# Kernel tuning notes

Measured on AMD Instinct MI355X. Metric: run time of the kernel, lower is better.

The kernel has to match this reference:

```python
import jax, jax.numpy as jnp
import numpy as np

DIM = 768
NUM_HEADS = 12
HEAD_DIM = DIM // NUM_HEADS
SCALE = HEAD_DIM ** -0.5


def setup_inputs() -> dict:
    key = jax.random.key(0)
    k_x, k_qw, k_qb, k_pw, k_pb = jax.random.split(key, 5)
    B, N = 4, 2048
    x = jax.random.normal(k_x, (B, N, DIM), dtype=jnp.float32)
    s = 1.0 / np.sqrt(DIM)
    qkv_w = jax.random.normal(k_qw, (3 * DIM, DIM), dtype=jnp.float32) * s
    qkv_b = jax.random.normal(k_qb, (3 * DIM,), dtype=jnp.float32) * 0.02
    proj_w = jax.random.normal(k_pw, (DIM, DIM), dtype=jnp.float32) * s
    proj_b = jax.random.normal(k_pb, (DIM,), dtype=jnp.float32) * 0.02
    return {"x": x, "qkv_w": qkv_w, "qkv_b": qkv_b, "proj_w": proj_w, "proj_b": proj_b}


def reference(x, qkv_w, qkv_b, proj_w, proj_b):
    B, N, D = x.shape
    H, Hd = NUM_HEADS, HEAD_DIM
    # qkv linear: [B,N,3D] -> [3,B,H,N,Hd]
    qkv = (x @ qkv_w.T + qkv_b).reshape(B, N, 3, H, Hd).transpose(2, 0, 3, 1, 4)
    q, k, v = qkv[0], qkv[1], qkv[2]
    scores = jnp.einsum("bhnd,bhmd->bhnm", q, k) * SCALE  # [B,H,N,N]
    attn = jax.nn.softmax(scores, axis=-1)
    out = jnp.einsum("bhnm,bhmd->bhnd", attn, v)  # [B,H,N,Hd]
    out = out.transpose(0, 2, 1, 3).reshape(B, N, D)
    return out @ proj_w.T + proj_b
```

## Files before the change

### kernel.cpp

```cpp
#include <hip/hip_runtime.h>

#define SEQ 2048
#define NB 4
#define NH 12
#define DHEAD 64
#define DMODEL 768
#define D3 2304
#define MTOT 8192
#define QSCALE 0.18033688011112042f

typedef float f4v __attribute__((ext_vector_type(4)));
typedef float fl4 __attribute__((ext_vector_type(4)));
typedef short s8v __attribute__((ext_vector_type(8)));
typedef __bf16 b8v __attribute__((ext_vector_type(8)));
typedef unsigned int ui4 __attribute__((ext_vector_type(4)));
typedef unsigned int ui2 __attribute__((ext_vector_type(2)));
typedef unsigned short us4 __attribute__((ext_vector_type(4)));

#define GLDS16(g, l)                                                            \
  __builtin_amdgcn_global_load_lds(                                             \
      (const __attribute__((address_space(1))) void*)(g),                       \
      (__attribute__((address_space(3))) void*)(l), 16, 0, 0)

__device__ inline float fast_exp2(float x) {
#if __has_builtin(__builtin_amdgcn_exp2f)
  return __builtin_amdgcn_exp2f(x);
#else
  float r;
  asm("v_exp_f32 %0, %1" : "=v"(r) : "v"(x));
  return r;
#endif
}

template <typename T>
__device__ inline auto mfma_try(T a, T b, f4v c, int)
    -> decltype(__builtin_amdgcn_mfma_f32_16x16x32_bf16(a, b, c, 0, 0, 0)) {
  return __builtin_amdgcn_mfma_f32_16x16x32_bf16(a, b, c, 0, 0, 0);
}
template <typename T>
__device__ inline f4v mfma_try(T a, T b, f4v c, long) {
  return __builtin_amdgcn_mfma_f32_16x16x32_bf16(
      __builtin_bit_cast(b8v, a), __builtin_bit_cast(b8v, b), c, 0, 0, 0);
}
__device__ inline f4v mfma16(s8v a, s8v b, f4v c) { return mfma_try(a, b, c, 0); }

__device__ inline unsigned short f2bf(float f) {
  union { float f; unsigned u; } v; v.f = f;
  unsigned r = v.u + 0x7FFFu + ((v.u >> 16) & 1u);
  return (unsigned short)(r >> 16);
}

__device__ inline unsigned pack2(float a, float b) {
  unsigned ua = __builtin_bit_cast(unsigned, a) + 0x8000u;
  unsigned ub = __builtin_bit_cast(unsigned, b) + 0x8000u;
  return __builtin_amdgcn_perm(ub, ua, 0x07060302u);
}

__device__ inline unsigned cvtpk2(float a, float b) {
  unsigned r;
  asm("v_cvt_pk_bf16_f32 %0, %1, %2" : "=v"(r) : "v"(a), "v"(b));
  return r;
}

#define NX4 1572864
#define NW14 442368
#define NW24 147456
__global__ void k_cvt(const float* __restrict__ x, const float* __restrict__ w1,
                      const float* __restrict__ w2, unsigned short* __restrict__ ox,
                      unsigned short* __restrict__ o1, unsigned short* __restrict__ o2) {
  int i = blockIdx.x * 256 + threadIdx.x;
  const float* src;
  unsigned short* dst;
  int off;
  if (i < NX4) { src = x; dst = ox; off = i; }
  else if (i < NX4 + NW14) { src = w1; dst = o1; off = i - NX4; }
  else if (i < NX4 + NW14 + NW24) { src = w2; dst = o2; off = i - NX4 - NW14; }
  else return;
  fl4 f = ((const fl4*)src)[off];
  ui2 o = ui2{cvtpk2(f[0], f[1]), cvtpk2(f[2], f[3])};
  ((ui2*)dst)[off] = o;
}

__global__ __launch_bounds__(256, 3) void k_qkv(
    const unsigned short* __restrict__ xb,
    const unsigned short* __restrict__ wb,
    const float* __restrict__ qkv_b,
    unsigned short* __restrict__ outQ,
    unsigned short* __restrict__ outK,
    unsigned short* __restrict__ outV) {
  __shared__ unsigned short As[128 * 64];
  __shared__ unsigned short Bs[128 * 64];
  const int tid = threadIdx.x;
  const int lane = tid & 63;
  const int wave = tid >> 6;
  const int wr = wave >> 1, wc = wave & 1;
  const int lr = lane & 15, lq = lane >> 4;
  const int srow = wave * 8 + (lane >> 3);
  const int scol = ((lane & 7) ^ ((lane >> 3) & 7)) * 8;
  const int swz = (lr & 7);

  const int bid = blockIdx.x;
  const int xcd = bid & 7;
  const int cc = bid >> 3;
  const int tokTile = xcd * 8 + cc / 24;
  const int rsel = cc % 24;

  if (rsel < 12) {
    const int rowBase = rsel * 128;
    const int colBase = tokTile * 128;
    f4v acc[4][4];
#pragma unroll
    for (int i = 0; i < 4; ++i)
#pragma unroll
      for (int j = 0; j < 4; ++j) acc[i][j] = f4v{0.f, 0.f, 0.f, 0.f};

    const unsigned short* Ag0 = wb + (long)(rowBase + srow) * DMODEL + scol;
    const unsigned short* Bg0 = xb + (long)(colBase + srow) * DMODEL + scol;
    unsigned short* Al0 = &As[srow * 64 + (lane & 7) * 8];
    unsigned short* Bl0 = &Bs[srow * 64 + (lane & 7) * 8];

    for (int kt = 0; kt < DMODEL / 64; ++kt) {
#pragma unroll
      for (int p = 0; p < 4; ++p) {
        GLDS16(Ag0 + kt * 64 + p * 32 * DMODEL, Al0 + p * 32 * 64);
        GLDS16(Bg0 + kt * 64 + p * 32 * DMODEL, Bl0 + p * 32 * 64);
      }
      __syncthreads();
#pragma unroll
      for (int ks = 0; ks < 2; ++ks) {
        s8v af[4], bf[4];
#pragma unroll
        for (int i = 0; i < 4; ++i)
          af[i] = *(const s8v*)&As[(wr * 64 + i * 16 + lr) * 64 + ((ks * 4 + lq) ^ swz) * 8];
#pragma unroll
        for (int j = 0; j < 4; ++j)
          bf[j] = *(const s8v*)&Bs[(wc * 64 + j * 16 + lr) * 64 + ((ks * 4 + lq) ^ swz) * 8];
#pragma unroll
        for (int i = 0; i < 4; ++i)
#pragma unroll
          for (int j = 0; j < 4; ++j) acc[i][j] = mfma16(af[i], bf[j], acc[i][j]);
      }
      __syncthreads();
    }

    const int fw = rowBase + wr * 64;
    fl4 bv[4];
#pragma unroll
    for (int i = 0; i < 4; ++i) bv[i] = *(const fl4*)&qkv_b[fw + i * 16 + lq * 4];
    const int isQ = fw < DMODEL;
    const int h = (fw >> 6) % NH;
    unsigned short* outQK = (unsigned short*)(isQ ? outQ : outK);
    const float scl = isQ ? QSCALE : 1.0f;
#pragma unroll
    for (int j = 0; j < 4; ++j) {
      const int ng = colBase + wc * 64 + j * 16 + lr;
      const int b = ng >> 11, nn = ng & 2047;
#pragma unroll
      for (int i = 0; i < 4; ++i) {
        float v0 = (acc[i][j][0] + bv[i][0]) * scl, v1 = (acc[i][j][1] + bv[i][1]) * scl;
        float v2 = (acc[i][j][2] + bv[i][2]) * scl, v3 = (acc[i][j][3] + bv[i][3]) * scl;
        *(ui2*)(outQK + (long)(((b * NH + h) * SEQ) + nn) * DHEAD + (i * 16 + lq * 4)) =
            ui2{cvtpk2(v0, v1), cvtpk2(v2, v3)};
      }
    }
  } else {
    const int rowBase = tokTile * 128;
    const int colBase = (rsel - 12) * 64;
    f4v acc[4][2];
#pragma unroll
    for (int i = 0; i < 4; ++i)
#pragma unroll
      for (int j = 0; j < 2; ++j) acc[i][j] = f4v{0.f, 0.f, 0.f, 0.f};

    const unsigned short* Ag0 = xb + (long)(rowBase + srow) * DMODEL + scol;
    const unsigned short* Bg0 =
        wb + (long)(2 * DMODEL + colBase + srow) * DMODEL + scol;
    unsigned short* Al0 = &As[srow * 64 + (lane & 7) * 8];
    unsigned short* Bl0 = &Bs[srow * 64 + (lane & 7) * 8];

    for (int kt = 0; kt < DMODEL / 64; ++kt) {
#pragma unroll
      for (int p = 0; p < 4; ++p)
        GLDS16(Ag0 + kt * 64 + p * 32 * DMODEL, Al0 + p * 32 * 64);
#pragma unroll
      for (int p = 0; p < 2; ++p)
        GLDS16(Bg0 + kt * 64 + p * 32 * DMODEL, Bl0 + p * 32 * 64);
      __syncthreads();
#pragma unroll
      for (int ks = 0; ks < 2; ++ks) {
        s8v af[4], bf[2];
#pragma unroll
        for (int i = 0; i < 4; ++i)
          af[i] = *(const s8v*)&As[(wr * 64 + i * 16 + lr) * 64 + ((ks * 4 + lq) ^ swz) * 8];
#pragma unroll
        for (int j = 0; j < 2; ++j)
          bf[j] = *(const s8v*)&Bs[(wc * 32 + j * 16 + lr) * 64 + ((ks * 4 + lq) ^ swz) * 8];
#pragma unroll
        for (int i = 0; i < 4; ++i)
#pragma unroll
          for (int j = 0; j < 2; ++j) acc[i][j] = mfma16(af[i], bf[j], acc[i][j]);
      }
      __syncthreads();
    }

#pragma unroll
    for (int j = 0; j < 2; ++j) {
      const int col = colBase + wc * 32 + j * 16 + lr;
      const float bvs = qkv_b[2 * DMODEL + col];
      const int h = col >> 6, hd = col & 63;
#pragma unroll
      for (int i = 0; i < 4; ++i) {
        const int row = rowBase + wr * 64 + i * 16 + lq * 4;
        const int b = row >> 11, n = row & 2047;
        const int bq = (n >> 2) & 7;
        const int np = (n & ~31) + ((bq & 3) << 3) + ((bq >> 2) << 2);
        float v0 = acc[i][j][0] + bvs, v1 = acc[i][j][1] + bvs;
        float v2 = acc[i][j][2] + bvs, v3 = acc[i][j][3] + bvs;
        *(ui2*)&outV[(long)(((b * NH + h) * DHEAD) + hd) * SEQ + np] =
            ui2{cvtpk2(v0, v1), cvtpk2(v2, v3)};
      }
    }
  }
}

__global__ __launch_bounds__(256, 3) void k_proj(
    const unsigned short* __restrict__ Wp,
    const unsigned short* __restrict__ Xt,
    const float* __restrict__ bias,
    float* __restrict__ outF) {
  __shared__ unsigned short As[128 * 64];
  __shared__ unsigned short Bs[64 * 64];
  const int tid = threadIdx.x;
  const int lane = tid & 63;
  const int wave = tid >> 6;
  const int wr = wave >> 1, wc = wave & 1;
  const int lr = lane & 15, lq = lane >> 4;
  const int srow = wave * 8 + (lane >> 3);
  const int scol = ((lane & 7) ^ ((lane >> 3) & 7)) * 8;
  const int swz = (lr & 7);

  const int bid = blockIdx.x;
  const int xcd = bid & 7;
  const int cc = bid >> 3;
  const int tokTile = xcd * 16 + cc / 6;
  const int rowBase = (cc % 6) * 128;
  const int colBase = tokTile * 64;

  f4v acc[4][2];
#pragma unroll
  for (int i = 0; i < 4; ++i)
#pragma unroll
    for (int j = 0; j < 2; ++j) acc[i][j] = f4v{0.f, 0.f, 0.f, 0.f};

  const unsigned short* Ag0 = Wp + (long)(rowBase + srow) * DMODEL + scol;
  const unsigned short* Bg0 = Xt + (long)(colBase + srow) * DMODEL + scol;
  unsigned short* Al0 = &As[srow * 64 + (lane & 7) * 8];
  unsigned short* Bl0 = &Bs[srow * 64 + (lane & 7) * 8];

  for (int kt = 0; kt < DMODEL / 64; ++kt) {
#pragma unroll
    for (int p = 0; p < 4; ++p)
      GLDS16(Ag0 + kt * 64 + p * 32 * DMODEL, Al0 + p * 32 * 64);
#pragma unroll
    for (int p = 0; p < 2; ++p)
      GLDS16(Bg0 + kt * 64 + p * 32 * DMODEL, Bl0 + p * 32 * 64);
    __syncthreads();
#pragma unroll
    for (int ks = 0; ks < 2; ++ks) {
      s8v af[4], bf[2];
#pragma unroll
      for (int i = 0; i < 4; ++i)
        af[i] = *(const s8v*)&As[(wr * 64 + i * 16 + lr) * 64 + ((ks * 4 + lq) ^ swz) * 8];
#pragma unroll
      for (int j = 0; j < 2; ++j)
        bf[j] = *(const s8v*)&Bs[(wc * 32 + j * 16 + lr) * 64 + ((ks * 4 + lq) ^ swz) * 8];
#pragma unroll
      for (int i = 0; i < 4; ++i)
#pragma unroll
        for (int j = 0; j < 2; ++j) acc[i][j] = mfma16(af[i], bf[j], acc[i][j]);
    }
    __syncthreads();
  }

  const int fw = rowBase + wr * 64;
  fl4 bv[4];
#pragma unroll
  for (int i = 0; i < 4; ++i) bv[i] = *(const fl4*)&bias[fw + i * 16 + lq * 4];
#pragma unroll
  for (int j = 0; j < 2; ++j) {
    const int ng = colBase + wc * 32 + j * 16 + lr;
#pragma unroll
    for (int i = 0; i < 4; ++i) {
      float v0 = acc[i][j][0] + bv[i][0], v1 = acc[i][j][1] + bv[i][1];
      float v2 = acc[i][j][2] + bv[i][2], v3 = acc[i][j][3] + bv[i][3];
      *(fl4*)&outF[(long)ng * DMODEL + fw + i * 16 + lq * 4] = fl4{v0, v1, v2, v3};
    }
  }
}

__global__ __launch_bounds__(256, 3) void k_attn(
    const unsigned short* __restrict__ Q,
    const unsigned short* __restrict__ Kg,
    const unsigned short* __restrict__ Vt,
    unsigned short* __restrict__ Ob) {
  __shared__ unsigned short Ks[2 * 128 * 64];
  __shared__ unsigned short Vs[64 * 128];
  const int tid = threadIdx.x;
  const int lane = tid & 63;
  const int wave = tid >> 6;
  const int lr = lane & 15;
  const int lq = lane >> 4;

  const int bid = blockIdx.x;
  const int xcd = bid & 7;
  const int cc = bid >> 3;
  const int bh = xcd * 6 + cc / 16;
  const int q0 = (cc & 15) * 128;

  const int b = bh / NH, h = bh % NH;
  const unsigned short* Qb = Q + (long)bh * SEQ * DHEAD;
  const unsigned short* Kb = Kg + (long)bh * SEQ * DHEAD;
  const unsigned short* Vb = Vt + (long)bh * DHEAD * SEQ;

  s8v qf[2][2];
#pragma unroll
  for (int i = 0; i < 2; ++i)
#pragma unroll
    for (int ss = 0; ss < 2; ++ss)
      qf[i][ss] = *(const s8v*)(Qb + (q0 + wave * 32 + i * 16 + lr) * DHEAD + ss * 32 + lq * 8);

  f4v o[2][4];
  f4v la[2] = {f4v{0.f, 0.f, 0.f, 0.f}, f4v{0.f, 0.f, 0.f, 0.f}};
  const f4v zc = f4v{0.f, 0.f, 0.f, 0.f};
  const s8v ones = {0x3F80, 0x3F80, 0x3F80, 0x3F80, 0x3F80, 0x3F80, 0x3F80, 0x3F80};
#pragma unroll
  for (int i = 0; i < 2; ++i)
#pragma unroll
    for (int jo = 0; jo < 4; ++jo) o[i][jo] = f4v{0.f, 0.f, 0.f, 0.f};

  const int srow = wave * 8 + (lane >> 3);
  const int scol = ((lane & 7) ^ ((lane >> 3) & 7)) * 8;
  const unsigned short* Kg0 = Kb + (long)srow * DHEAD + scol;
  const int klBase = srow * 64 + (lane & 7) * 8;
  const int swz = (lr & 7);
  const int vdrow = wave * 4 + (lane >> 4);
  const int vchunk = (lane & 15) ^ vdrow;
  const unsigned short* Vg0 = Vb + (long)vdrow * SEQ + vchunk * 8;
  unsigned short* Vl0 = &Vs[vdrow * 128 + (lane & 15) * 8];

#pragma unroll
  for (int p = 0; p < 4; ++p)
    GLDS16(Kg0 + (long)(p * 32) * DHEAD, &Ks[klBase] + p * 32 * 64);
  __syncthreads();

  int cur = 0;
  for (int kt = 0; kt < SEQ / 128; ++kt) {
#pragma unroll
    for (int p = 0; p < 4; ++p)
      GLDS16(Vg0 + (long)(p * 16) * SEQ + kt * 128, Vl0 + p * 16 * 128);
    if (kt + 1 < SEQ / 128) {
#pragma unroll
      for (int p = 0; p < 4; ++p)
        GLDS16(Kg0 + (long)((kt + 1) * 128 + p * 32) * DHEAD,
               &Ks[(cur ^ 1) * (128 * 64) + klBase] + p * 32 * 64);
    }

    const unsigned short* Kc = &Ks[cur * (128 * 64)];
    f4v s[2][8];
    __builtin_amdgcn_s_setprio(1);
#pragma unroll
    for (int t = 0; t < 8; ++t) {
      s8v kf0 = *(const s8v*)&Kc[(t * 16 + lr) * 64 + ((0 * 4 + lq) ^ swz) * 8];
      s8v kf1 = *(const s8v*)&Kc[(t * 16 + lr) * 64 + ((1 * 4 + lq) ^ swz) * 8];
      s[0][t] = mfma16(kf0, qf[0][0], zc);
      s[1][t] = mfma16(kf0, qf[1][0], zc);
      s[0][t] = mfma16(kf1, qf[0][1], s[0][t]);
      s[1][t] = mfma16(kf1, qf[1][1], s[1][t]);
    }
    __builtin_amdgcn_s_setprio(0);

    unsigned pk[2][8][2];
#pragma unroll
    for (int i = 0; i < 2; ++i)
#pragma unroll
      for (int t = 0; t < 4; ++t) {
        float p0 = fast_exp2(s[i][t][0]);
        float p1 = fast_exp2(s[i][t][1]);
        float p2 = fast_exp2(s[i][t][2]);
        float p3 = fast_exp2(s[i][t][3]);
        pk[i][t][0] = cvtpk2(p0, p1);
        pk[i][t][1] = cvtpk2(p2, p3);
      }

    __syncthreads();

#pragma unroll
    for (int ss = 0; ss < 4; ++ss) {
      s8v vf[4];
#pragma unroll
      for (int jo = 0; jo < 4; ++jo)
        vf[jo] = *(const s8v*)&Vs[(jo * 16 + lr) * 128 + ((ss * 4 + lq) ^ lr) * 8];
      __builtin_amdgcn_s_setprio(1);
#pragma unroll
      for (int i = 0; i < 2; ++i) {
        s8v pf = __builtin_bit_cast(
            s8v, ui4{pk[i][2 * ss][0], pk[i][2 * ss][1], pk[i][2 * ss + 1][0], pk[i][2 * ss + 1][1]});
        la[i] = mfma16(ones, pf, la[i]);
#pragma unroll
        for (int jo = 0; jo < 4; ++jo) o[i][jo] = mfma16(vf[jo], pf, o[i][jo]);
      }
      __builtin_amdgcn_s_setprio(0);
      if (ss < 2) {
#pragma unroll
        for (int i = 0; i < 2; ++i)
#pragma unroll
          for (int t = 4 + 2 * ss; t < 6 + 2 * ss; ++t) {
            float p0 = fast_exp2(s[i][t][0]);
            float p1 = fast_exp2(s[i][t][1]);
            float p2 = fast_exp2(s[i][t][2]);
            float p3 = fast_exp2(s[i][t][3]);
            pk[i][t][0] = cvtpk2(p0, p1);
            pk[i][t][1] = cvtpk2(p2, p3);
          }
      }
    }

    __syncthreads();
    cur ^= 1;
  }

  float linv[2];
  linv[0] = 1.0f / la[0][0];
  linv[1] = 1.0f / la[1][0];

#pragma unroll
  for (int i = 0; i < 2; ++i) {
    const long nrow = (long)(b * SEQ + q0 + wave * 32 + i * 16 + lr) * DMODEL;
#pragma unroll
    for (int jo = 0; jo < 4; ++jo) {
      float v0 = o[i][jo][0] * linv[i];
      float v1 = o[i][jo][1] * linv[i];
      float v2 = o[i][jo][2] * linv[i];
      float v3 = o[i][jo][3] * linv[i];
      *(ui2*)(Ob + nrow + h * DHEAD + jo * 16 + lq * 4) = ui2{cvtpk2(v0, v1), cvtpk2(v2, v3)};
    }
  }
}

extern "C" void kernel_launch(void* const* d_in, const int* in_sizes, int n_in,
                              void* d_out, int out_size, void* d_ws, size_t ws_size,
                              hipStream_t stream) {
  (void)in_sizes; (void)n_in; (void)out_size; (void)ws_size;
  const float* x = (const float*)d_in[0];
  const float* qkv_w = (const float*)d_in[1];
  const float* qkv_b = (const float*)d_in[2];
  const float* proj_w = (const float*)d_in[3];
  const float* proj_b = (const float*)d_in[4];
  float* out = (float*)d_out;

  unsigned short* ws = (unsigned short*)d_ws;
  unsigned short* xb = ws;
  unsigned short* wqkvb = xb + 6291456;
  unsigned short* wprjb = wqkvb + 1769472;
  unsigned short* qb = wprjb + 589824;
  unsigned short* kb = qb + 6291456;
  unsigned short* vtb = kb + 6291456;
  unsigned short* aob = vtb + 6291456;

  k_cvt<<<(NX4 + NW14 + NW24 + 255) / 256, 256, 0, stream>>>(
      x, qkv_w, proj_w, xb, wqkvb, wprjb);

  k_qkv<<<1536, 256, 0, stream>>>(xb, wqkvb, qkv_b, qb, kb, vtb);
  k_attn<<<768, 256, 0, stream>>>(qb, kb, vtb, aob);
  k_proj<<<768, 256, 0, stream>>>(wprjb, aob, proj_b, out);
}
```

Measured before the change: 195.3 us.

## Fuse V projection into QK blocks of QKV GEMM sharing the x tile

The QKV kernel used to launch separate blocks for the Q/K part and the V part, and both loaded the same x tile. Each block now computes one 128x128 Q/K tile and also a 128x64 V tile, reusing the x tile already staged in LDS as the A operand for V. This halves the grid and avoids loading x twice. In exchange each block holds more accumulator registers and an extra LDS buffer, which may reduce occupancy below the 3 blocks per CU requested by the launch bounds.

After: 196.6 us. About the same (+0.7%).

```diff
diff --git a/kernel.cpp b/kernel.cpp
--- a/kernel.cpp
+++ b/kernel.cpp
@@ -90,6 +90,7 @@
     unsigned short* __restrict__ outV) {
   __shared__ unsigned short As[128 * 64];
   __shared__ unsigned short Bs[128 * 64];
+  __shared__ unsigned short Cs[64 * 64];
   const int tid = threadIdx.x;
   const int lane = tid & 63;
   const int wave = tid >> 6;
@@ -102,47 +103,68 @@
   const int bid = blockIdx.x;
   const int xcd = bid & 7;
   const int cc = bid >> 3;
-  const int tokTile = xcd * 8 + cc / 24;
-  const int rsel = cc % 24;
-
-  if (rsel < 12) {
-    const int rowBase = rsel * 128;
-    const int colBase = tokTile * 128;
-    f4v acc[4][4];
-#pragma unroll
-    for (int i = 0; i < 4; ++i)
-#pragma unroll
-      for (int j = 0; j < 4; ++j) acc[i][j] = f4v{0.f, 0.f, 0.f, 0.f};
-
-    const unsigned short* Ag0 = wb + (long)(rowBase + srow) * DMODEL + scol;
-    const unsigned short* Bg0 = xb + (long)(colBase + srow) * DMODEL + scol;
-    unsigned short* Al0 = &As[srow * 64 + (lane & 7) * 8];
-    unsigned short* Bl0 = &Bs[srow * 64 + (lane & 7) * 8];
-
-    for (int kt = 0; kt < DMODEL / 64; ++kt) {
-#pragma unroll
-      for (int p = 0; p < 4; ++p) {
-        GLDS16(Ag0 + kt * 64 + p * 32 * DMODEL, Al0 + p * 32 * 64);
-        GLDS16(Bg0 + kt * 64 + p * 32 * DMODEL, Bl0 + p * 32 * 64);
-      }
-      __syncthreads();
-#pragma unroll
-      for (int ks = 0; ks < 2; ++ks) {
-        s8v af[4], bf[4];
-#pragma unroll
-        for (int i = 0; i < 4; ++i)
-          af[i] = *(const s8v*)&As[(wr * 64 + i * 16 + lr) * 64 + ((ks * 4 + lq) ^ swz) * 8];
-#pragma unroll
-        for (int j = 0; j < 4; ++j)
-          bf[j] = *(const s8v*)&Bs[(wc * 64 + j * 16 + lr) * 64 + ((ks * 4 + lq) ^ swz) * 8];
-#pragma unroll
-        for (int i = 0; i < 4; ++i)
-#pragma unroll
-          for (int j = 0; j < 4; ++j) acc[i][j] = mfma16(af[i], bf[j], acc[i][j]);
-      }
-      __syncthreads();
-    }
-
+  const int tokTile = xcd * 8 + cc / 12;
+  const int rsel = cc % 12;
+
+  const int rowBase = rsel * 128;
+  const int colBase = tokTile * 128;
+  const int vColBase = rsel * 64;
+
+  f4v acc[4][4];
+  f4v accv[4][2];
+#pragma unroll
+  for (int i = 0; i < 4; ++i) {
+#pragma unroll
+    for (int j = 0; j < 4; ++j) acc[i][j] = f4v{0.f, 0.f, 0.f, 0.f};
+#pragma unroll
+    for (int j = 0; j < 2; ++j) accv[i][j] = f4v{0.f, 0.f, 0.f, 0.f};
+  }
+
+  const unsigned short* Ag0 = wb + (long)(rowBase + srow) * DMODEL + scol;
+  const unsigned short* Bg0 = xb + (long)(colBase + srow) * DMODEL + scol;
+  const unsigned short* Cg0 = wb + (long)(2 * DMODEL + vColBase + srow) * DMODEL + scol;
+  unsigned short* Al0 = &As[srow * 64 + (lane & 7) * 8];
+  unsigned short* Bl0 = &Bs[srow * 64 + (lane & 7) * 8];
+  unsigned short* Cl0 = &Cs[srow * 64 + (lane & 7) * 8];
+
+  for (int kt = 0; kt < DMODEL / 64; ++kt) {
+#pragma unroll
+    for (int p = 0; p < 4; ++p) {
+      GLDS16(Ag0 + kt * 64 + p * 32 * DMODEL, Al0 + p * 32 * 64);
+      GLDS16(Bg0 + kt * 64 + p * 32 * DMODEL, Bl0 + p * 32 * 64);
+    }
+#pragma unroll
+    for (int p = 0; p < 2; ++p)
+      GLDS16(Cg0 + kt * 64 + p * 32 * DMODEL, Cl0 + p * 32 * 64);
+    __syncthreads();
+#pragma unroll
+    for (int ks = 0; ks < 2; ++ks) {
+      const int kcol = ((ks * 4 + lq) ^ swz) * 8;
+      s8v bf[4];
+#pragma unroll
+      for (int j = 0; j < 4; ++j)
+        bf[j] = *(const s8v*)&Bs[(wc * 64 + j * 16 + lr) * 64 + kcol];
+#pragma unroll
+      for (int i = 0; i < 4; ++i) {
+        s8v af = *(const s8v*)&As[(wr * 64 + i * 16 + lr) * 64 + kcol];
+#pragma unroll
+        for (int j = 0; j < 4; ++j) acc[i][j] = mfma16(af, bf[j], acc[i][j]);
+      }
+      s8v cvf[2];
+#pragma unroll
+      for (int j = 0; j < 2; ++j)
+        cvf[j] = *(const s8v*)&Cs[(wc * 32 + j * 16 + lr) * 64 + kcol];
+#pragma unroll
+      for (int i = 0; i < 4; ++i) {
+        s8v avf = *(const s8v*)&Bs[(wr * 64 + i * 16 + lr) * 64 + kcol];
+#pragma unroll
+        for (int j = 0; j < 2; ++j) accv[i][j] = mfma16(avf, cvf[j], accv[i][j]);
+      }
+    }
+    __syncthreads();
+  }
+
+  {
     const int fw = rowBase + wr * 64;
     fl4 bv[4];
 #pragma unroll
@@ -163,62 +185,23 @@
             ui2{cvtpk2(v0, v1), cvtpk2(v2, v3)};
       }
     }
-  } else {
-    const int rowBase = tokTile * 128;
-    const int colBase = (rsel - 12) * 64;
-    f4v acc[4][2];
-#pragma unroll
-    for (int i = 0; i < 4; ++i)
-#pragma unroll
-      for (int j = 0; j < 2; ++j) acc[i][j] = f4v{0.f, 0.f, 0.f, 0.f};
-
-    const unsigned short* Ag0 = xb + (long)(rowBase + srow) * DMODEL + scol;
-    const unsigned short* Bg0 =
-        wb + (long)(2 * DMODEL + colBase + srow) * DMODEL + scol;
-    unsigned short* Al0 = &As[srow * 64 + (lane & 7) * 8];
-    unsigned short* Bl0 = &Bs[srow * 64 + (lane & 7) * 8];
-
-    for (int kt = 0; kt < DMODEL / 64; ++kt) {
-#pragma unroll
-      for (int p = 0; p < 4; ++p)
-        GLDS16(Ag0 + kt * 64 + p * 32 * DMODEL, Al0 + p * 32 * 64);
-#pragma unroll
-      for (int p = 0; p < 2; ++p)
-        GLDS16(Bg0 + kt * 64 + p * 32 * DMODEL, Bl0 + p * 32 * 64);
-      __syncthreads();
-#pragma unroll
-      for (int ks = 0; ks < 2; ++ks) {
-        s8v af[4], bf[2];
-#pragma unroll
-        for (int i = 0; i < 4; ++i)
-          af[i] = *(const s8v*)&As[(wr * 64 + i * 16 + lr) * 64 + ((ks * 4 + lq) ^ swz) * 8];
-#pragma unroll
-        for (int j = 0; j < 2; ++j)
-          bf[j] = *(const s8v*)&Bs[(wc * 32 + j * 16 + lr) * 64 + ((ks * 4 + lq) ^ swz) * 8];
-#pragma unroll
-        for (int i = 0; i < 4; ++i)
-#pragma unroll
-          for (int j = 0; j < 2; ++j) acc[i][j] = mfma16(af[i], bf[j], acc[i][j]);
-      }
-      __syncthreads();
-    }
-
-#pragma unroll
-    for (int j = 0; j < 2; ++j) {
-      const int col = colBase + wc * 32 + j * 16 + lr;
-      const float bvs = qkv_b[2 * DMODEL + col];
-      const int h = col >> 6, hd = col & 63;
-#pragma unroll
-      for (int i = 0; i < 4; ++i) {
-        const int row = rowBase + wr * 64 + i * 16 + lq * 4;
-        const int b = row >> 11, n = row & 2047;
-        const int bq = (n >> 2) & 7;
-        const int np = (n & ~31) + ((bq & 3) << 3) + ((bq >> 2) << 2);
-        float v0 = acc[i][j][0] + bvs, v1 = acc[i][j][1] + bvs;
-        float v2 = acc[i][j][2] + bvs, v3 = acc[i][j][3] + bvs;
-        *(ui2*)&outV[(long)(((b * NH + h) * DHEAD) + hd) * SEQ + np] =
-            ui2{cvtpk2(v0, v1), cvtpk2(v2, v3)};
-      }
+  }
+
+#pragma unroll
+  for (int j = 0; j < 2; ++j) {
+    const int col = vColBase + wc * 32 + j * 16 + lr;
+    const float bvs = qkv_b[2 * DMODEL + col];
+    const int h = col >> 6, hd = col & 63;
+#pragma unroll
+    for (int i = 0; i < 4; ++i) {
+      const int row = colBase + wr * 64 + i * 16 + lq * 4;
+      const int b = row >> 11, n = row & 2047;
+      const int bq = (n >> 2) & 7;
+      const int np = (n & ~31) + ((bq & 3) << 3) + ((bq >> 2) << 2);
+      float v0 = accv[i][j][0] + bvs, v1 = accv[i][j][1] + bvs;
+      float v2 = accv[i][j][2] + bvs, v3 = accv[i][j][3] + bvs;
+      *(ui2*)&outV[(long)(((b * NH + h) * DHEAD) + hd) * SEQ + np] =
+          ui2{cvtpk2(v0, v1), cvtpk2(v2, v3)};
     }
   }
 }
@@ -470,7 +453,7 @@
   k_cvt<<<(NX4 + NW14 + NW24 + 255) / 256, 256, 0, stream>>>(
       x, qkv_w, proj_w, xb, wqkvb, wprjb);
 
-  k_qkv<<<1536, 256, 0, stream>>>(xb, wqkvb, qkv_b, qb, kb, vtb);
+  k_qkv<<<768, 256, 0, stream>>>(xb, wqkvb, qkv_b, qb, kb, vtb);
   k_attn<<<768, 256, 0, stream>>>(qb, kb, vtb, aob);
   k_proj<<<768, 256, 0, stream>>>(wprjb, aob, proj_b, out);
 }
```
